# Kernel optimization log

Hardware: AMD Instinct MI355X
Metric: run time of the kernel (lower is better)

## Reference

```python
import jax, jax.numpy as jnp
import numpy as np

N = 30000   # nodes
E = 600000  # edges (avg degree 20)
H = 128     # hidden_channels
L = 4       # num_layers
G = 64      # graphs in batch


def _init(key, shape, fan_in):
    return (jax.random.normal(key, shape, jnp.float32) / np.sqrt(fan_in)).astype(jnp.float32)


def setup_inputs() -> dict:
    key = jax.random.key(0)
    ks = jax.random.split(key, 24)
    x = jax.random.normal(ks[0], (N, 1), jnp.float32)
    pos = jax.random.normal(ks[1], (N, 3), jnp.float32)
    edge_index = jax.random.randint(ks[2], (2, E), 0, N, dtype=jnp.int32).astype(jnp.int64)
    batch = jnp.sort(jax.random.randint(ks[3], (N,), 0, G, dtype=jnp.int32)).astype(jnp.int64)

    emb_w = _init(ks[4], (1, H), 1)
    emb_b = jnp.zeros((H,), jnp.float32)

    # stacked per-layer params: msg MLP (2H+1 -> H -> H), node MLP (2H -> H -> H)
    msg_w1 = _init(ks[5], (L, 2 * H + 1, H), 2 * H + 1)
    msg_b1 = jnp.zeros((L, H), jnp.float32)
    msg_w2 = _init(ks[6], (L, H, H), H)
    msg_b2 = jnp.zeros((L, H), jnp.float32)
    node_w1 = _init(ks[7], (L, 2 * H, H), 2 * H)
    node_b1 = jnp.zeros((L, H), jnp.float32)
    node_w2 = _init(ks[8], (L, H, H), H)
    node_b2 = jnp.zeros((L, H), jnp.float32)

    out_w1 = _init(ks[9], (H, 32), H)
    out_b1 = jnp.zeros((32,), jnp.float32)
    out_w2 = _init(ks[10], (32, 1), 32)
    out_b2 = jnp.zeros((1,), jnp.float32)

    return {
        "x": x, "pos": pos, "edge_index": edge_index, "batch": batch,
        "emb_w": emb_w, "emb_b": emb_b,
        "msg_w1": msg_w1, "msg_b1": msg_b1, "msg_w2": msg_w2, "msg_b2": msg_b2,
        "node_w1": node_w1, "node_b1": node_b1, "node_w2": node_w2, "node_b2": node_b2,
        "out_w1": out_w1, "out_b1": out_b1, "out_w2": out_w2, "out_b2": out_b2,
    }


def reference(x, pos, edge_index, batch,
              emb_w, emb_b,
              msg_w1, msg_b1, msg_w2, msg_b2,
              node_w1, node_b1, node_w2, node_b2,
              out_w1, out_b1, out_w2, out_b2):
    row, col = edge_index[0], edge_index[1]  # row = source j, col = target i
    # edge scalar: squared distance (computed once, reused across layers)
    dist_sq = jnp.sum((pos[row] - pos[col]) ** 2, axis=-1, keepdims=True)  # [E,1]

    h = x @ emb_w + emb_b  # [N,H]
    for l in range(L):
        x_j = h[row]   # source features
        x_i = h[col]   # target features
        m = jnp.concatenate([x_i, x_j, dist_sq], axis=-1)           # [E, 2H+1]
        m = jax.nn.silu(m @ msg_w1[l] + msg_b1[l]) @ msg_w2[l] + msg_b2[l]  # [E,H]
        aggr = jax.ops.segment_sum(m, col, num_segments=N)          # scatter-add to targets
        nh = jnp.concatenate([h, aggr], axis=-1)                    # [N, 2H]
        h = jax.nn.silu(nh @ node_w1[l] + node_b1[l]) @ node_w2[l] + node_b2[l]
        # dropout omitted for deterministic reference (eval mode)

    g = jax.ops.segment_sum(h, batch, num_segments=G)               # global_add_pool [G,H]
    return jax.nn.silu(g @ out_w1 + out_b1) @ out_w2 + out_b2       # [G,1]
```

## Files before the change

### kernel.cpp

```cpp
#include <hip/hip_runtime.h>

typedef unsigned short u16;
typedef __bf16 bf16x8 __attribute__((ext_vector_type(8)));
typedef float f32x4 __attribute__((ext_vector_type(4)));

#define HN 128
#define TM 64
#define ASTRIDE 136
#define ECH 256
#define PGRID 256

__device__ __forceinline__ u16 f2bf(float f) {
  union { float f; unsigned u; } v; v.f = f;
  unsigned r = v.u + 0x7fffu + ((v.u >> 16) & 1u);
  return (u16)(r >> 16);
}
__device__ __forceinline__ float bf2f(u16 v) {
  union { unsigned u; float f; } x; x.u = ((unsigned)v) << 16; return x.f;
}
__device__ __forceinline__ float bflo(unsigned v) {
  union { unsigned u; float f; } x; x.u = v << 16; return x.f;
}
__device__ __forceinline__ float bfhi(unsigned v) {
  union { unsigned u; float f; } x; x.u = v & 0xffff0000u; return x.f;
}
__device__ __forceinline__ float silu_f(float x) {
  float e = __builtin_amdgcn_exp2f(-1.442695041f * x);
  return x * __builtin_amdgcn_rcpf(1.f + e);
}

__global__ void pack_weights(const float* __restrict__ msg_w1, const float* __restrict__ msg_w2,
                             const float* __restrict__ node_w1, const float* __restrict__ node_w2,
                             u16* __restrict__ pw, int* __restrict__ deg,
                             float* __restrict__ g, int N_, int GH) {
  int id = blockIdx.x * 256 + threadIdx.x;
  if (id < N_) deg[id] = 0;
  if (id < GH) g[id] = 0.f;
  if (id >= 4 * 6 * 16384) return;
  int l = id / (6 * 16384);
  int rem = id % (6 * 16384);
  int m = rem / 16384;
  int e = rem % 16384;
  int kg = e >> 10;
  int n = (e >> 3) & 127;
  int j = e & 7;
  int k = kg * 8 + j;
  float v = 0.f;
  switch (m) {
    case 0: v = msg_w1[(l * 257 + k) * 128 + n]; break;
    case 1: v = msg_w1[(l * 257 + 128 + k) * 128 + n]; break;
    case 2: v = msg_w2[(l * 128 + k) * 128 + n]; break;
    case 3: v = node_w1[(l * 256 + k) * 128 + n]; break;
    case 4: v = node_w1[(l * 256 + 128 + k) * 128 + n]; break;
    case 5: v = node_w2[(l * 128 + k) * 128 + n]; break;
  }
  pw[id] = f2bf(v);
}

__device__ __forceinline__ void gemm64(const u16* s_A, const u16* s_W,
                                       int w, int quad, int m16, f32x4 acc[8]) {
#pragma unroll
  for (int ks = 0; ks < 4; ks++) {
    bf16x8 a = *(const bf16x8*)&s_A[(w * 16 + m16) * ASTRIDE + ks * 32 + quad * 8];
#pragma unroll
    for (int ct = 0; ct < 8; ct++) {
      bf16x8 b = *(const bf16x8*)&s_W[(ks * 4 + quad) * 1024 + (ct * 16 + m16) * 8];
      acc[ct] = __builtin_amdgcn_mfma_f32_16x16x32_bf16(a, b, acc[ct], 0, 0, 0);
    }
  }
}

__device__ __forceinline__ void gemm64_ra(const bf16x8 aH[4], const u16* s_W,
                                          int quad, int m16, f32x4 acc[8]) {
#pragma unroll
  for (int ks = 0; ks < 4; ks++) {
#pragma unroll
    for (int ct = 0; ct < 8; ct++) {
      bf16x8 b = *(const bf16x8*)&s_W[(ks * 4 + quad) * 1024 + (ct * 16 + m16) * 8];
      acc[ct] = __builtin_amdgcn_mfma_f32_16x16x32_bf16(aH[ks], b, acc[ct], 0, 0, 0);
    }
  }
}

__device__ __forceinline__ void gemm64_gb(const u16* s_A, const u16* __restrict__ gW,
                                          int w, int quad, int m16, f32x4 acc[8]) {
#pragma unroll
  for (int ks = 0; ks < 4; ks++) {
    bf16x8 a = *(const bf16x8*)&s_A[(w * 16 + m16) * ASTRIDE + ks * 32 + quad * 8];
#pragma unroll
    for (int ct = 0; ct < 8; ct++) {
      bf16x8 b = *(const bf16x8*)&gW[(ks * 4 + quad) * 1024 + (ct * 16 + m16) * 8];
      acc[ct] = __builtin_amdgcn_mfma_f32_16x16x32_bf16(a, b, acc[ct], 0, 0, 0);
    }
  }
}

__global__ __launch_bounds__(256) void fold_kernel(
    const float* __restrict__ msg_w2, const float* __restrict__ node_w1,
    const float* __restrict__ msg_b2, const u16* __restrict__ pw,
    u16* __restrict__ pwc, float* __restrict__ vc) {
  __shared__ __align__(16) u16 s_A[TM * ASTRIDE];
  __shared__ __align__(16) u16 s_W[16384];
  const int t = threadIdx.x;
  const int w = t >> 6, lane = t & 63, quad = lane >> 4, m16 = lane & 15;
  const int b = blockIdx.x, l = b >> 1, half = b & 1;
  const int tile0 = half * 64;

  {
    int r = t >> 2, qo = (t & 3) * 32;
    const float4* src = (const float4*)(msg_w2 + (size_t)(l * 128 + tile0 + r) * 128 + qo);
    u16* dst = s_A + r * ASTRIDE + qo;
#pragma unroll
    for (int i = 0; i < 8; i++) {
      float4 v = src[i];
      ushort4 o;
      o.x = f2bf(v.x); o.y = f2bf(v.y); o.z = f2bf(v.z); o.w = f2bf(v.w);
      *(ushort4*)(dst + i * 4) = o;
    }
  }
  {
    const int4* src = (const int4*)(pw + (size_t)(l * 6 + 4) * 16384);
    int4* dst = (int4*)s_W;
#pragma unroll
    for (int i = 0; i < 8; i++) dst[t + i * 256] = src[t + i * 256];
  }
  __syncthreads();
  f32x4 acc[8];
#pragma unroll
  for (int ct = 0; ct < 8; ct++) acc[ct] = {0.f, 0.f, 0.f, 0.f};
  gemm64(s_A, s_W, w, quad, m16, acc);
#pragma unroll
  for (int ct = 0; ct < 8; ct++)
#pragma unroll
    for (int j = 0; j < 4; j++) {
      int k = tile0 + w * 16 + quad * 4 + j;
      int n = ct * 16 + m16;
      pwc[(size_t)l * 16384 + (k >> 3) * 1024 + n * 8 + (k & 7)] = f2bf(acc[ct][j]);
    }
  if (half == 0 && t < 128) {
    float s = 0.f;
    for (int np = 0; np < 128; np++)
      s += msg_b2[l * 128 + np] * node_w1[(size_t)(l * 256 + 128 + np) * 128 + t];
    vc[l * 128 + t] = s;
  }
}

__global__ void hist_kernel(const int* __restrict__ eidx, int* __restrict__ deg,
                            int* __restrict__ rnk, int E_) {
  int e = blockIdx.x * 256 + threadIdx.x;
  if (e < E_) rnk[e] = atomicAdd(&deg[eidx[E_ + e]], 1);
}

__global__ void scan1_kernel(const int* __restrict__ deg, int* __restrict__ off,
                             int* __restrict__ bsum, int n) {
  __shared__ int s[256];
  int t = threadIdx.x;
  int i = blockIdx.x * 256 + t;
  int v = (i < n) ? deg[i] : 0;
  s[t] = v;
  for (int d = 1; d < 256; d <<= 1) {
    __syncthreads();
    int x = (t >= d) ? s[t - d] : 0;
    __syncthreads();
    s[t] += x;
  }
  __syncthreads();
  if (i < n) off[i] = s[t] - v;
  if (t == 255) bsum[blockIdx.x] = s[255];
}

__global__ void scan2_kernel(int* __restrict__ bsum, int nb) {
  __shared__ int s[256];
  int t = threadIdx.x;
  int v = (t < nb) ? bsum[t] : 0;
  s[t] = v;
  for (int d = 1; d < 256; d <<= 1) {
    __syncthreads();
    int x = (t >= d) ? s[t - d] : 0;
    __syncthreads();
    s[t] += x;
  }
  __syncthreads();
  if (t < nb) bsum[t] = s[t] - v;
}

__global__ void scan3_kernel(int* __restrict__ off, const int* __restrict__ bsum, int n) {
  int i = blockIdx.x * 256 + threadIdx.x;
  if (i < n) off[i] += bsum[blockIdx.x];
}

__global__ void scatter_kernel(const int* __restrict__ eidx, const float* __restrict__ pos,
                               const int* __restrict__ off, const int* __restrict__ rnk,
                               int2* __restrict__ es8, int E_) {
  int e = blockIdx.x * 256 + threadIdx.x;
  if (e >= E_) return;
  int sr = eidx[e], tg = eidx[E_ + e];
  float dx = pos[sr * 3 + 0] - pos[tg * 3 + 0];
  float dy = pos[sr * 3 + 1] - pos[tg * 3 + 1];
  float dz = pos[sr * 3 + 2] - pos[tg * 3 + 2];
  float d = dx * dx + dy * dy + dz * dz;
  int p = off[tg] + rnk[e];
  int2 v;
  v.x = sr | (tg << 15);
  v.y = __float_as_int(d);
  es8[p] = v;
}

__global__ __launch_bounds__(256, 1) void proj_kernel(
    const float* __restrict__ x, const float* __restrict__ emb_w,
    const float* __restrict__ emb_b, u16* __restrict__ hbf,
    u16* __restrict__ Pout, u16* __restrict__ Qout,
    const u16* __restrict__ pw, const float* __restrict__ b1,
    float* __restrict__ S, int NH4, int nnodes, int ntiles) {
  __shared__ __align__(16) u16 s_W[2 * 16384];
  const int t = threadIdx.x;
  const int w = t >> 6, lane = t & 63, quad = lane >> 4, m16 = lane & 15;

  {
    float4* S4 = (float4*)S;
    int id = blockIdx.x * 256 + t;
    int stride = PGRID * 256;
    float4 z = {0.f, 0.f, 0.f, 0.f};
    for (int i = id; i < NH4; i += stride) S4[i] = z;
  }
  {
    const int4* src0 = (const int4*)pw;
    const int4* src1 = (const int4*)(pw + 16384);
    int4* dst = (int4*)s_W;
#pragma unroll
    for (int i = 0; i < 8; i++) dst[t + i * 256] = src0[t + i * 256];
#pragma unroll
    for (int i = 0; i < 8; i++) dst[2048 + t + i * 256] = src1[t + i * 256];
  }
  float ew[4][8], eb[4][8], bb[8];
#pragma unroll
  for (int ks = 0; ks < 4; ks++)
#pragma unroll
    for (int i = 0; i < 8; i++) {
      int c = ks * 32 + quad * 8 + i;
      ew[ks][i] = emb_w[c];
      eb[ks][i] = emb_b[c];
    }
#pragma unroll
  for (int ct = 0; ct < 8; ct++) bb[ct] = b1[ct * 16 + m16];
  __syncthreads();

  for (int tile = blockIdx.x; tile < ntiles; tile += PGRID) {
    const int tile0 = tile * TM;
    int nodem = tile0 + w * 16 + m16;
    bool live = nodem < nnodes;
    if (!live) nodem = nnodes - 1;
    float xv = x[nodem];
    bf16x8 aH[4];
#pragma unroll
    for (int ks = 0; ks < 4; ks++) {
      u16 hv[8];
#pragma unroll
      for (int i = 0; i < 8; i++) hv[i] = f2bf(xv * ew[ks][i] + eb[ks][i]);
      aH[ks] = *(bf16x8*)hv;
      if (live) *(int4*)&hbf[(size_t)nodem * HN + ks * 32 + quad * 8] = *(int4*)hv;
    }
    f32x4 acc[8];
#pragma unroll
    for (int ct = 0; ct < 8; ct++) acc[ct] = {0.f, 0.f, 0.f, 0.f};
    gemm64_ra(aH, s_W, quad, m16, acc);
#pragma unroll
    for (int ct = 0; ct < 8; ct++)
#pragma unroll
      for (int j = 0; j < 4; j++) {
        int n = tile0 + w * 16 + quad * 4 + j;
        if (n < nnodes) Pout[(size_t)n * HN + ct * 16 + m16] = f2bf(acc[ct][j] + bb[ct]);
      }
#pragma unroll
    for (int ct = 0; ct < 8; ct++) acc[ct] = {0.f, 0.f, 0.f, 0.f};
    gemm64_ra(aH, s_W + 16384, quad, m16, acc);
#pragma unroll
    for (int ct = 0; ct < 8; ct++)
#pragma unroll
      for (int j = 0; j < 4; j++) {
        int n = tile0 + w * 16 + quad * 4 + j;
        if (n < nnodes) Qout[(size_t)n * HN + ct * 16 + m16] = f2bf(acc[ct][j]);
      }
  }
}

__device__ __forceinline__ void edge_step(
    int tg_s, float dd_s, unsigned qv,
    int& cur_s, float& p0, float& p1, float& s0, float& s1,
    const u16* __restrict__ P, float* __restrict__ S, int cp,
    float wd0, float wd1, int tprev_s, int tnext_s) {
  if (tg_s != cur_s) {
    if (cur_s >= 0) {
      float* dst = &S[(size_t)cur_s * HN + cp];
      if (cur_s == tprev_s || cur_s == tnext_s) {
        atomicAdd(dst, s0);
        atomicAdd(dst + 1, s1);
      } else {
        float2 v = {s0, s1};
        *(float2*)dst = v;
      }
    }
    cur_s = tg_s; s0 = 0.f; s1 = 0.f;
    int cg = tg_s < 0 ? 0 : tg_s;
    unsigned pv = *(const unsigned*)&P[(size_t)cg * HN + cp];
    p0 = bflo(pv); p1 = bfhi(pv);
  }
  float x0 = p0 + bflo(qv) + dd_s * wd0;
  float x1 = p1 + bfhi(qv) + dd_s * wd1;
  s0 += silu_f(x0);
  s1 += silu_f(x1);
}

__global__ __launch_bounds__(256) void edge_kernel(
    const u16* __restrict__ P, const u16* __restrict__ Q,
    float* __restrict__ S, const float* __restrict__ w1d,
    const int2* __restrict__ es8, int E_) {
  __shared__ int s_src[ECH + 8];
  __shared__ int s_tgt[ECH + 8];
  __shared__ float s_dist[ECH + 8];

  const int t = threadIdx.x;
  const int e0 = blockIdx.x * ECH;
  {
    int e = e0 + t;
    if (e < E_) {
      int2 v = es8[e];
      s_src[t] = v.x & 0x7fff;
      s_tgt[t] = v.x >> 15;
      s_dist[t] = __int_as_float(v.y);
    } else {
      s_src[t] = 0; s_tgt[t] = -1; s_dist[t] = 0.f;
    }
    if (t < 8) { s_src[ECH + t] = 0; s_tgt[ECH + t] = -1; s_dist[ECH + t] = 0.f; }
  }
  __syncthreads();

  const int lane = t & 63;
  const int w = t >> 6;
  const int cp = lane * 2;
  const int a = w * 64;
  const float2 wdv = *(const float2*)&w1d[cp];
  const float wd0 = wdv.x, wd1 = wdv.y;

  int tprev_s, tnext_s;
  if (w == 0) tprev_s = (e0 > 0) ? (es8[e0 - 1].x >> 15) : -2;
  else tprev_s = s_tgt[a - 1];
  if (w == 3) tnext_s = (e0 + ECH < E_) ? (es8[e0 + ECH].x >> 15) : -2;
  else tnext_s = s_tgt[a + 64];
  tprev_s = __builtin_amdgcn_readfirstlane(tprev_s);
  tnext_s = __builtin_amdgcn_readfirstlane(tnext_s);

  int tg[8];
  float dd[8];
  unsigned qv[8];
#pragma unroll
  for (int j = 0; j < 8; j++) {
    tg[j] = s_tgt[a + j];
    dd[j] = s_dist[a + j];
    qv[j] = *(const unsigned*)&Q[(size_t)s_src[a + j] * HN + cp];
  }

  int cur_s = -1;
  float s0 = 0.f, s1 = 0.f, p0 = 0.f, p1 = 0.f;

#pragma unroll
  for (int i = a; i < a + 64; i += 8) {
    int tgn[8];
    float ddn[8];
    unsigned qvn[8];
#pragma unroll
    for (int j = 0; j < 8; j++) {
      int idx = i + 8 + j;
      tgn[j] = s_tgt[idx];
      ddn[j] = s_dist[idx];
      qvn[j] = *(const unsigned*)&Q[(size_t)s_src[idx] * HN + cp];
    }
#pragma unroll
    for (int j = 0; j < 8; j++) {
      int tg_s = __builtin_amdgcn_readfirstlane(tg[j]);
      edge_step(tg_s, dd[j], qv[j], cur_s, p0, p1, s0, s1, P, S, cp, wd0, wd1, tprev_s, tnext_s);
    }
#pragma unroll
    for (int j = 0; j < 8; j++) { tg[j] = tgn[j]; dd[j] = ddn[j]; qv[j] = qvn[j]; }
  }

  if (cur_s >= 0) {
    float* dst = &S[(size_t)cur_s * HN + cp];
    if (cur_s == tprev_s || cur_s == tnext_s) {
      atomicAdd(dst, s0);
      atomicAdd(dst + 1, s1);
    } else {
      float2 v = {s0, s1};
      *(float2*)dst = v;
    }
  }
}

template <bool FUSE>
__global__ __launch_bounds__(256, 1) void node_kernel(
    const u16* __restrict__ hbf, float* __restrict__ S, const int* __restrict__ deg,
    u16* __restrict__ hout, const u16* __restrict__ pwc, const float* __restrict__ vc,
    const u16* __restrict__ pwn, const float* __restrict__ b1, const float* __restrict__ b2,
    const u16* __restrict__ pw_next, const float* __restrict__ b1_next,
    u16* __restrict__ Pout, u16* __restrict__ Qout, int nnodes, int ntiles) {
  __shared__ __align__(16) u16 s_A[TM * ASTRIDE];
  __shared__ __align__(16) u16 s_W[(FUSE ? 4 : 3) * 16384];
  const int t = threadIdx.x;
  const int w = t >> 6, lane = t & 63, quad = lane >> 4, m16 = lane & 15;
  const int r_ = t >> 2, qo_ = (t & 3) * 32;

  {
    const int4* src0 = (const int4*)pwc;
    const int4* src1 = (const int4*)pwn;
    const int4* src2 = (const int4*)(pwn + 32768);
    int4* dst = (int4*)s_W;
#pragma unroll
    for (int i = 0; i < 8; i++) dst[t + i * 256] = src0[t + i * 256];
#pragma unroll
    for (int i = 0; i < 8; i++) dst[2048 + t + i * 256] = src1[t + i * 256];
#pragma unroll
    for (int i = 0; i < 8; i++) dst[4096 + t + i * 256] = src2[t + i * 256];
    if (FUSE) {
      const int4* src3 = (const int4*)pw_next;
#pragma unroll
      for (int i = 0; i < 8; i++) dst[6144 + t + i * 256] = src3[t + i * 256];
    }
  }
  float bb1[8], vcr[8], bb2[8], bbn[8];
#pragma unroll
  for (int ct = 0; ct < 8; ct++) {
    bb1[ct] = b1[ct * 16 + m16];
    vcr[ct] = vc[ct * 16 + m16];
    bb2[ct] = b2[ct * 16 + m16];
    bbn[ct] = FUSE ? b1_next[ct * 16 + m16] : 0.f;
  }
  __syncthreads();

  for (int tile = blockIdx.x; tile < ntiles; tile += PGRID) {
    const int tile0 = tile * TM;
    int node_ = tile0 + r_;
    if (node_ >= nnodes) node_ = nnodes - 1;
    int nodem = tile0 + w * 16 + m16;
    if (nodem >= nnodes) nodem = nnodes - 1;

    {
      const float4* src = (const float4*)(S + (size_t)node_ * HN + qo_);
      u16* dst = s_A + r_ * ASTRIDE + qo_;
#pragma unroll
      for (int i = 0; i < 8; i++) {
        float4 v = src[i];
        ushort4 o;
        o.x = f2bf(v.x); o.y = f2bf(v.y); o.z = f2bf(v.z); o.w = f2bf(v.w);
        *(ushort4*)(dst + i * 4) = o;
      }
      float4 z = {0.f, 0.f, 0.f, 0.f};
      float4* zd = (float4*)(S + (size_t)node_ * HN + qo_);
#pragma unroll
      for (int i = 0; i < 8; i++) zd[i] = z;
    }
    asm volatile("s_waitcnt lgkmcnt(0)" ::: "memory");

    f32x4 acc[8];
#pragma unroll
    for (int ct = 0; ct < 8; ct++) acc[ct] = {0.f, 0.f, 0.f, 0.f};
    gemm64(s_A, s_W, w, quad, m16, acc);

    bf16x8 aH[4];
#pragma unroll
    for (int ks = 0; ks < 4; ks++)
      aH[ks] = *(const bf16x8*)&hbf[(size_t)nodem * HN + ks * 32 + quad * 8];
    gemm64_ra(aH, s_W + 16384, quad, m16, acc);

    {
      float degv[4];
#pragma unroll
      for (int j = 0; j < 4; j++) {
        int n = tile0 + w * 16 + quad * 4 + j;
        if (n >= nnodes) n = nnodes - 1;
        degv[j] = (float)deg[n];
      }
#pragma unroll
      for (int ct = 0; ct < 8; ct++)
#pragma unroll
        for (int j = 0; j < 4; j++) {
          int row = w * 16 + quad * 4 + j;
          float xv = acc[ct][j] + bb1[ct] + degv[j] * vcr[ct];
          s_A[row * ASTRIDE + ct * 16 + m16] = f2bf(silu_f(xv));
        }
    }
    asm volatile("s_waitcnt lgkmcnt(0)" ::: "memory");

#pragma unroll
    for (int ct = 0; ct < 8; ct++) acc[ct] = {0.f, 0.f, 0.f, 0.f};
    gemm64(s_A, s_W + 32768, w, quad, m16, acc);

#pragma unroll
    for (int ct = 0; ct < 8; ct++)
#pragma unroll
      for (int j = 0; j < 4; j++) {
        int row = w * 16 + quad * 4 + j;
        int n = tile0 + row;
        u16 hv = f2bf(acc[ct][j] + bb2[ct]);
        if (n < nnodes) hout[(size_t)n * HN + ct * 16 + m16] = hv;
        if (FUSE) s_A[row * ASTRIDE + ct * 16 + m16] = hv;
      }

    if (FUSE) {
      asm volatile("s_waitcnt lgkmcnt(0)" ::: "memory");
#pragma unroll
      for (int ct = 0; ct < 8; ct++) acc[ct] = {0.f, 0.f, 0.f, 0.f};
      gemm64(s_A, s_W + 49152, w, quad, m16, acc);
#pragma unroll
      for (int ct = 0; ct < 8; ct++)
#pragma unroll
        for (int j = 0; j < 4; j++) {
          int n = tile0 + w * 16 + quad * 4 + j;
          if (n < nnodes) Pout[(size_t)n * HN + ct * 16 + m16] = f2bf(acc[ct][j] + bbn[ct]);
        }
#pragma unroll
      for (int ct = 0; ct < 8; ct++) acc[ct] = {0.f, 0.f, 0.f, 0.f};
      gemm64_gb(s_A, pw_next + 16384, w, quad, m16, acc);
#pragma unroll
      for (int ct = 0; ct < 8; ct++)
#pragma unroll
        for (int j = 0; j < 4; j++) {
          int n = tile0 + w * 16 + quad * 4 + j;
          if (n < nnodes) Qout[(size_t)n * HN + ct * 16 + m16] = f2bf(acc[ct][j]);
        }
    }
  }
}

__global__ __launch_bounds__(256) void pool_kernel(
    const u16* __restrict__ h, const int* __restrict__ batch,
    float* __restrict__ g, int N) {
  __shared__ int s_b[64];
  const int t = threadIdx.x;
  const int n0 = blockIdx.x * 64;
  if (t < 64) {
    int n = n0 + t;
    s_b[t] = (n < N) ? batch[n] : -1;
  }
  __syncthreads();
  const int cp = (t & 63) * 2;
  const int rg = t >> 6;
  int cur = -1;
  float s0 = 0.f, s1 = 0.f;
#pragma unroll 4
  for (int i = 0; i < 16; i++) {
    int r = rg * 16 + i;
    int b = s_b[r];
    if (b < 0) break;
    if (b != cur) {
      if (cur >= 0) {
        atomicAdd(&g[cur * HN + cp], s0);
        atomicAdd(&g[cur * HN + cp + 1], s1);
      }
      cur = b; s0 = 0.f; s1 = 0.f;
    }
    unsigned v = *(const unsigned*)&h[(size_t)(n0 + r) * HN + cp];
    s0 += bf2f((u16)(v & 0xffffu));
    s1 += bf2f((u16)(v >> 16));
  }
  if (cur >= 0) {
    atomicAdd(&g[cur * HN + cp], s0);
    atomicAdd(&g[cur * HN + cp + 1], s1);
  }
}

__global__ __launch_bounds__(64) void out_kernel(
    const float* __restrict__ g, const float* __restrict__ w1,
    const float* __restrict__ b1, const float* __restrict__ w2,
    const float* __restrict__ b2, float* __restrict__ out) {
  const int gi = blockIdx.x;
  const int t = threadIdx.x;
  const int c = t & 31, kh = t >> 5;
  float s = 0.f;
  for (int k = kh * 64; k < kh * 64 + 64; k++)
    s += g[gi * HN + k] * w1[k * 32 + c];
  s += __shfl_down(s, 32);
  float r = 0.f;
  if (kh == 0) r = silu_f(s + b1[c]) * w2[c];
  r += __shfl_down(r, 16);
  r += __shfl_down(r, 8);
  r += __shfl_down(r, 4);
  r += __shfl_down(r, 2);
  r += __shfl_down(r, 1);
  if (t == 0) out[gi] = r + b2[0];
}

extern "C" void kernel_launch(void* const* d_in, const int* in_sizes, int n_in,
                              void* d_out, int out_size, void* d_ws, size_t ws_size,
                              hipStream_t stream) {
  const float* x = (const float*)d_in[0];
  const float* pos = (const float*)d_in[1];
  const int* eidx = (const int*)d_in[2];
  const int* batch = (const int*)d_in[3];
  const float* emb_w = (const float*)d_in[4];
  const float* emb_b = (const float*)d_in[5];
  const float* msg_w1 = (const float*)d_in[6];
  const float* msg_b1 = (const float*)d_in[7];
  const float* msg_w2 = (const float*)d_in[8];
  const float* msg_b2 = (const float*)d_in[9];
  const float* node_w1 = (const float*)d_in[10];
  const float* node_b1 = (const float*)d_in[11];
  const float* node_w2 = (const float*)d_in[12];
  const float* node_b2 = (const float*)d_in[13];
  const float* out_w1 = (const float*)d_in[14];
  const float* out_b1 = (const float*)d_in[15];
  const float* out_w2 = (const float*)d_in[16];
  const float* out_b2 = (const float*)d_in[17];
  float* outp = (float*)d_out;

  const int N = 30000, E = 600000, G = 64;
  const size_t NH = (size_t)N * HN;

  u16* hA = (u16*)d_ws;
  u16* hB = hA + NH;
  u16* Pp = hB + NH;
  u16* Qp = Pp + NH;
  float* S = (float*)(Qp + NH);
  int2* es8 = (int2*)(S + NH);
  int* deg = (int*)(es8 + E);
  int* off = deg + N;
  int* bsum = off + N;
  float* g = (float*)(bsum + 128);
  u16* pw = (u16*)(g + G * HN);
  u16* pwc = pw + (size_t)4 * 6 * 16384;
  float* vcb = (float*)(pwc + (size_t)4 * 16384);
  int* rnk = (int*)S;

  const int NB = (N + 255) / 256;
  const int NTB = (N + TM - 1) / TM;

  pack_weights<<<(4 * 6 * 16384 + 255) / 256, 256, 0, stream>>>(
      msg_w1, msg_w2, node_w1, node_w2, pw, deg, g, N, G * HN);
  fold_kernel<<<8, 256, 0, stream>>>(msg_w2, node_w1, msg_b2, pw, pwc, vcb);

  hist_kernel<<<(E + 255) / 256, 256, 0, stream>>>(eidx, deg, rnk, E);
  scan1_kernel<<<NB, 256, 0, stream>>>(deg, off, bsum, N);
  scan2_kernel<<<1, 256, 0, stream>>>(bsum, NB);
  scan3_kernel<<<NB, 256, 0, stream>>>(off, bsum, N);
  scatter_kernel<<<(E + 255) / 256, 256, 0, stream>>>(eidx, pos, off, rnk, es8, E);

  proj_kernel<<<PGRID, 256, 0, stream>>>(x, emb_w, emb_b, hA, Pp, Qp, pw, msg_b1,
                                         S, (int)(NH / 4), N, NTB);

  u16* hcur = hA;
  u16* hnext = hB;
  for (int l = 0; l < 4; l++) {
    const u16* pwl = pw + (size_t)(l * 6) * 16384;
    edge_kernel<<<(E + ECH - 1) / ECH, 256, 0, stream>>>(
        Pp, Qp, S,
        msg_w1 + (size_t)(l * 257 + 256) * 128,
        es8, E);
    if (l < 3) {
      const u16* pw_next = pw + (size_t)((l + 1) * 6) * 16384;
      node_kernel<true><<<PGRID, 256, 0, stream>>>(
          hcur, S, deg, hnext, pwc + (size_t)l * 16384, vcb + l * 128,
          pwl + 3 * 16384, node_b1 + l * 128, node_b2 + l * 128,
          pw_next, msg_b1 + (l + 1) * 128, Pp, Qp, N, NTB);
    } else {
      node_kernel<false><<<PGRID, 256, 0, stream>>>(
          hcur, S, deg, hnext, pwc + (size_t)l * 16384, vcb + l * 128,
          pwl + 3 * 16384, node_b1 + l * 128, node_b2 + l * 128,
          nullptr, nullptr, nullptr, nullptr, N, NTB);
    }
    u16* tmp = hcur; hcur = hnext; hnext = tmp;
  }

  pool_kernel<<<(N + 63) / 64, 256, 0, stream>>>(hcur, batch, g, N);
  out_kernel<<<G, 64, 0, stream>>>(g, out_w1, out_b1, out_w2, out_b2, outp);
}
```

Baseline: 420.2 us.

## Read weights from global memory and launch one block per node tile

Measured after the change: 413.5 us. Within noise of the previous version (-1.6%).

```diff
diff --git a/kernel.cpp b/kernel.cpp
--- a/kernel.cpp
+++ b/kernel.cpp
@@ -8,7 +8,6 @@
 #define TM 64
 #define ASTRIDE 136
 #define ECH 256
-#define PGRID 256
 
 __device__ __forceinline__ u16 f2bf(float f) {
   union { float f; unsigned u; } v; v.f = f;
@@ -70,18 +69,6 @@
   }
 }
 
-__device__ __forceinline__ void gemm64_ra(const bf16x8 aH[4], const u16* s_W,
-                                          int quad, int m16, f32x4 acc[8]) {
-#pragma unroll
-  for (int ks = 0; ks < 4; ks++) {
-#pragma unroll
-    for (int ct = 0; ct < 8; ct++) {
-      bf16x8 b = *(const bf16x8*)&s_W[(ks * 4 + quad) * 1024 + (ct * 16 + m16) * 8];
-      acc[ct] = __builtin_amdgcn_mfma_f32_16x16x32_bf16(aH[ks], b, acc[ct], 0, 0, 0);
-    }
-  }
-}
-
 __device__ __forceinline__ void gemm64_gb(const u16* s_A, const u16* __restrict__ gW,
                                           int w, int quad, int m16, f32x4 acc[8]) {
 #pragma unroll
@@ -91,6 +78,18 @@
     for (int ct = 0; ct < 8; ct++) {
       bf16x8 b = *(const bf16x8*)&gW[(ks * 4 + quad) * 1024 + (ct * 16 + m16) * 8];
       acc[ct] = __builtin_amdgcn_mfma_f32_16x16x32_bf16(a, b, acc[ct], 0, 0, 0);
+    }
+  }
+}
+
+__device__ __forceinline__ void gemm64_ra_gb(const bf16x8 aH[4], const u16* __restrict__ gW,
+                                             int quad, int m16, f32x4 acc[8]) {
+#pragma unroll
+  for (int ks = 0; ks < 4; ks++) {
+#pragma unroll
+    for (int ct = 0; ct < 8; ct++) {
+      bf16x8 b = *(const bf16x8*)&gW[(ks * 4 + quad) * 1024 + (ct * 16 + m16) * 8];
+      acc[ct] = __builtin_amdgcn_mfma_f32_16x16x32_bf16(aH[ks], b, acc[ct], 0, 0, 0);
     }
   }
 }
@@ -206,82 +205,65 @@
   es8[p] = v;
 }
 
-__global__ __launch_bounds__(256, 1) void proj_kernel(
+__global__ __launch_bounds__(256) void proj_kernel(
     const float* __restrict__ x, const float* __restrict__ emb_w,
     const float* __restrict__ emb_b, u16* __restrict__ hbf,
     u16* __restrict__ Pout, u16* __restrict__ Qout,
     const u16* __restrict__ pw, const float* __restrict__ b1,
-    float* __restrict__ S, int NH4, int nnodes, int ntiles) {
-  __shared__ __align__(16) u16 s_W[2 * 16384];
+    float* __restrict__ S, int NH4, int nblocks, int nnodes) {
   const int t = threadIdx.x;
   const int w = t >> 6, lane = t & 63, quad = lane >> 4, m16 = lane & 15;
+  const int tile0 = blockIdx.x * TM;
 
   {
     float4* S4 = (float4*)S;
     int id = blockIdx.x * 256 + t;
-    int stride = PGRID * 256;
+    int stride = nblocks * 256;
     float4 z = {0.f, 0.f, 0.f, 0.f};
     for (int i = id; i < NH4; i += stride) S4[i] = z;
   }
-  {
-    const int4* src0 = (const int4*)pw;
-    const int4* src1 = (const int4*)(pw + 16384);
-    int4* dst = (int4*)s_W;
-#pragma unroll
-    for (int i = 0; i < 8; i++) dst[t + i * 256] = src0[t + i * 256];
-#pragma unroll
-    for (int i = 0; i < 8; i++) dst[2048 + t + i * 256] = src1[t + i * 256];
-  }
-  float ew[4][8], eb[4][8], bb[8];
-#pragma unroll
-  for (int ks = 0; ks < 4; ks++)
+
+  int nodem = tile0 + w * 16 + m16;
+  bool live = nodem < nnodes;
+  if (!live) nodem = nnodes - 1;
+  float xv = x[nodem];
+  bf16x8 aH[4];
+#pragma unroll
+  for (int ks = 0; ks < 4; ks++) {
+    u16 hv[8];
 #pragma unroll
     for (int i = 0; i < 8; i++) {
       int c = ks * 32 + quad * 8 + i;
-      ew[ks][i] = emb_w[c];
-      eb[ks][i] = emb_b[c];
-    }
+      hv[i] = f2bf(xv * emb_w[c] + emb_b[c]);
+    }
+    aH[ks] = *(bf16x8*)hv;
+    if (live) *(int4*)&hbf[(size_t)nodem * HN + ks * 32 + quad * 8] = *(int4*)hv;
+  }
+  float bb[8];
 #pragma unroll
   for (int ct = 0; ct < 8; ct++) bb[ct] = b1[ct * 16 + m16];
-  __syncthreads();
-
-  for (int tile = blockIdx.x; tile < ntiles; tile += PGRID) {
-    const int tile0 = tile * TM;
-    int nodem = tile0 + w * 16 + m16;
-    bool live = nodem < nnodes;
-    if (!live) nodem = nnodes - 1;
-    float xv = x[nodem];
-    bf16x8 aH[4];
-#pragma unroll
-    for (int ks = 0; ks < 4; ks++) {
-      u16 hv[8];
-#pragma unroll
-      for (int i = 0; i < 8; i++) hv[i] = f2bf(xv * ew[ks][i] + eb[ks][i]);
-      aH[ks] = *(bf16x8*)hv;
-      if (live) *(int4*)&hbf[(size_t)nodem * HN + ks * 32 + quad * 8] = *(int4*)hv;
-    }
-    f32x4 acc[8];
-#pragma unroll
-    for (int ct = 0; ct < 8; ct++) acc[ct] = {0.f, 0.f, 0.f, 0.f};
-    gemm64_ra(aH, s_W, quad, m16, acc);
-#pragma unroll
-    for (int ct = 0; ct < 8; ct++)
-#pragma unroll
-      for (int j = 0; j < 4; j++) {
-        int n = tile0 + w * 16 + quad * 4 + j;
-        if (n < nnodes) Pout[(size_t)n * HN + ct * 16 + m16] = f2bf(acc[ct][j] + bb[ct]);
-      }
-#pragma unroll
-    for (int ct = 0; ct < 8; ct++) acc[ct] = {0.f, 0.f, 0.f, 0.f};
-    gemm64_ra(aH, s_W + 16384, quad, m16, acc);
-#pragma unroll
-    for (int ct = 0; ct < 8; ct++)
-#pragma unroll
-      for (int j = 0; j < 4; j++) {
-        int n = tile0 + w * 16 + quad * 4 + j;
-        if (n < nnodes) Qout[(size_t)n * HN + ct * 16 + m16] = f2bf(acc[ct][j]);
-      }
-  }
+
+  f32x4 acc[8];
+#pragma unroll
+  for (int ct = 0; ct < 8; ct++) acc[ct] = {0.f, 0.f, 0.f, 0.f};
+  gemm64_ra_gb(aH, pw, quad, m16, acc);
+#pragma unroll
+  for (int ct = 0; ct < 8; ct++)
+#pragma unroll
+    for (int j = 0; j < 4; j++) {
+      int n = tile0 + w * 16 + quad * 4 + j;
+      if (n < nnodes) Pout[(size_t)n * HN + ct * 16 + m16] = f2bf(acc[ct][j] + bb[ct]);
+    }
+#pragma unroll
+  for (int ct = 0; ct < 8; ct++) acc[ct] = {0.f, 0.f, 0.f, 0.f};
+  gemm64_ra_gb(aH, pw + 16384, quad, m16, acc);
+#pragma unroll
+  for (int ct = 0; ct < 8; ct++)
+#pragma unroll
+    for (int j = 0; j < 4; j++) {
+      int n = tile0 + w * 16 + quad * 4 + j;
+      if (n < nnodes) Qout[(size_t)n * HN + ct * 16 + m16] = f2bf(acc[ct][j]);
+    }
 }
 
 __device__ __forceinline__ void edge_step(
@@ -397,35 +379,25 @@
 }
 
 template <bool FUSE>
-__global__ __launch_bounds__(256, 1) void node_kernel(
+__global__ __launch_bounds__(256) void node_kernel(
     const u16* __restrict__ hbf, float* __restrict__ S, const int* __restrict__ deg,
     u16* __restrict__ hout, const u16* __restrict__ pwc, const float* __restrict__ vc,
     const u16* __restrict__ pwn, const float* __restrict__ b1, const float* __restrict__ b2,
     const u16* __restrict__ pw_next, const float* __restrict__ b1_next,
-    u16* __restrict__ Pout, u16* __restrict__ Qout, int nnodes, int ntiles) {
+    u16* __restrict__ Pout, u16* __restrict__ Qout, int nnodes) {
   __shared__ __align__(16) u16 s_A[TM * ASTRIDE];
-  __shared__ __align__(16) u16 s_W[(FUSE ? 4 : 3) * 16384];
   const int t = threadIdx.x;
   const int w = t >> 6, lane = t & 63, quad = lane >> 4, m16 = lane & 15;
-  const int r_ = t >> 2, qo_ = (t & 3) * 32;
-
-  {
-    const int4* src0 = (const int4*)pwc;
-    const int4* src1 = (const int4*)pwn;
-    const int4* src2 = (const int4*)(pwn + 32768);
-    int4* dst = (int4*)s_W;
-#pragma unroll
-    for (int i = 0; i < 8; i++) dst[t + i * 256] = src0[t + i * 256];
-#pragma unroll
-    for (int i = 0; i < 8; i++) dst[2048 + t + i * 256] = src1[t + i * 256];
-#pragma unroll
-    for (int i = 0; i < 8; i++) dst[4096 + t + i * 256] = src2[t + i * 256];
-    if (FUSE) {
-      const int4* src3 = (const int4*)pw_next;
-#pragma unroll
-      for (int i = 0; i < 8; i++) dst[6144 + t + i * 256] = src3[t + i * 256];
-    }
-  }
+  const int tile0 = blockIdx.x * TM;
+  const int rb = lane >> 2;
+  const int qo = (lane & 3) * 32;
+  u16* band = s_A + (w * 16) * ASTRIDE;
+
+  int node_ = tile0 + w * 16 + rb;
+  if (node_ >= nnodes) node_ = nnodes - 1;
+  int nodem = tile0 + w * 16 + m16;
+  if (nodem >= nnodes) nodem = nnodes - 1;
+
   float bb1[8], vcr[8], bb2[8], bbn[8];
 #pragma unroll
   for (int ct = 0; ct < 8; ct++) {
@@ -434,100 +406,94 @@
     bb2[ct] = b2[ct * 16 + m16];
     bbn[ct] = FUSE ? b1_next[ct * 16 + m16] : 0.f;
   }
-  __syncthreads();
-
-  for (int tile = blockIdx.x; tile < ntiles; tile += PGRID) {
-    const int tile0 = tile * TM;
-    int node_ = tile0 + r_;
-    if (node_ >= nnodes) node_ = nnodes - 1;
-    int nodem = tile0 + w * 16 + m16;
-    if (nodem >= nnodes) nodem = nnodes - 1;
-
-    {
-      const float4* src = (const float4*)(S + (size_t)node_ * HN + qo_);
-      u16* dst = s_A + r_ * ASTRIDE + qo_;
-#pragma unroll
-      for (int i = 0; i < 8; i++) {
-        float4 v = src[i];
-        ushort4 o;
-        o.x = f2bf(v.x); o.y = f2bf(v.y); o.z = f2bf(v.z); o.w = f2bf(v.w);
-        *(ushort4*)(dst + i * 4) = o;
+
+  {
+    const float4* src = (const float4*)(S + (size_t)node_ * HN + qo);
+    u16* dst = band + rb * ASTRIDE + qo;
+#pragma unroll
+    for (int i = 0; i < 8; i++) {
+      float4 v = src[i];
+      ushort4 o;
+      o.x = f2bf(v.x); o.y = f2bf(v.y); o.z = f2bf(v.z); o.w = f2bf(v.w);
+      *(ushort4*)(dst + i * 4) = o;
+    }
+    float4 z = {0.f, 0.f, 0.f, 0.f};
+    float4* zd = (float4*)(S + (size_t)node_ * HN + qo);
+#pragma unroll
+    for (int i = 0; i < 8; i++) zd[i] = z;
+  }
+  asm volatile("s_waitcnt lgkmcnt(0)" ::: "memory");
+  __builtin_amdgcn_sched_barrier(0);
+
+  f32x4 acc[8];
+#pragma unroll
+  for (int ct = 0; ct < 8; ct++) acc[ct] = {0.f, 0.f, 0.f, 0.f};
+  gemm64_gb(s_A, pwc, w, quad, m16, acc);
+
+  bf16x8 aH[4];
+#pragma unroll
+  for (int ks = 0; ks < 4; ks++)
+    aH[ks] = *(const bf16x8*)&hbf[(size_t)nodem * HN + ks * 32 + quad * 8];
+  gemm64_ra_gb(aH, pwn, quad, m16, acc);
+
+  {
+    float degv[4];
+#pragma unroll
+    for (int j = 0; j < 4; j++) {
+      int n = tile0 + w * 16 + quad * 4 + j;
+      if (n >= nnodes) n = nnodes - 1;
+      degv[j] = (float)deg[n];
+    }
+#pragma unroll
+    for (int ct = 0; ct < 8; ct++)
+#pragma unroll
+      for (int j = 0; j < 4; j++) {
+        int row = quad * 4 + j;
+        float xv = acc[ct][j] + bb1[ct] + degv[j] * vcr[ct];
+        band[row * ASTRIDE + ct * 16 + m16] = f2bf(silu_f(xv));
       }
-      float4 z = {0.f, 0.f, 0.f, 0.f};
-      float4* zd = (float4*)(S + (size_t)node_ * HN + qo_);
-#pragma unroll
-      for (int i = 0; i < 8; i++) zd[i] = z;
-    }
+  }
+  asm volatile("s_waitcnt lgkmcnt(0)" ::: "memory");
+  __builtin_amdgcn_sched_barrier(0);
+
+#pragma unroll
+  for (int ct = 0; ct < 8; ct++) acc[ct] = {0.f, 0.f, 0.f, 0.f};
+  gemm64_gb(s_A, pwn + 32768, w, quad, m16, acc);
+
+#pragma unroll
+  for (int ct = 0; ct < 8; ct++)
+#pragma unroll
+    for (int j = 0; j < 4; j++) {
+      int row = quad * 4 + j;
+      int n = tile0 + w * 16 + row;
+      u16 hv = f2bf(acc[ct][j] + bb2[ct]);
+      if (n < nnodes) hout[(size_t)n * HN + ct * 16 + m16] = hv;
+      if (FUSE) band[row * ASTRIDE + ct * 16 + m16] = hv;
+    }
+
+  if (FUSE) {
     asm volatile("s_waitcnt lgkmcnt(0)" ::: "memory");
-
-    f32x4 acc[8];
+    __builtin_amdgcn_sched_barrier(0);
 #pragma unroll
     for (int ct = 0; ct < 8; ct++) acc[ct] = {0.f, 0.f, 0.f, 0.f};
-    gemm64(s_A, s_W, w, quad, m16, acc);
-
-    bf16x8 aH[4];
-#pragma unroll
-    for (int ks = 0; ks < 4; ks++)
-      aH[ks] = *(const bf16x8*)&hbf[(size_t)nodem * HN + ks * 32 + quad * 8];
-    gemm64_ra(aH, s_W + 16384, quad, m16, acc);
-
-    {
-      float degv[4];
+    gemm64_gb(s_A, pw_next, w, quad, m16, acc);
+#pragma unroll
+    for (int ct = 0; ct < 8; ct++)
 #pragma unroll
       for (int j = 0; j < 4; j++) {
         int n = tile0 + w * 16 + quad * 4 + j;
-        if (n >= nnodes) n = nnodes - 1;
-        degv[j] = (float)deg[n];
+        if (n < nnodes) Pout[(size_t)n * HN + ct * 16 + m16] = f2bf(acc[ct][j] + bbn[ct]);
       }
 #pragma unroll
-      for (int ct = 0; ct < 8; ct++)
-#pragma unroll
-        for (int j = 0; j < 4; j++) {
-          int row = w * 16 + quad * 4 + j;
-          float xv = acc[ct][j] + bb1[ct] + degv[j] * vcr[ct];
-          s_A[row * ASTRIDE + ct * 16 + m16] = f2bf(silu_f(xv));
-        }
-    }
-    asm volatile("s_waitcnt lgkmcnt(0)" ::: "memory");
-
-#pragma unroll
     for (int ct = 0; ct < 8; ct++) acc[ct] = {0.f, 0.f, 0.f, 0.f};
-    gemm64(s_A, s_W + 32768, w, quad, m16, acc);
-
+    gemm64_gb(s_A, pw_next + 16384, w, quad, m16, acc);
 #pragma unroll
     for (int ct = 0; ct < 8; ct++)
 #pragma unroll
       for (int j = 0; j < 4; j++) {
-        int row = w * 16 + quad * 4 + j;
-        int n = tile0 + row;
-        u16 hv = f2bf(acc[ct][j] + bb2[ct]);
-        if (n < nnodes) hout[(size_t)n * HN + ct * 16 + m16] = hv;
-        if (FUSE) s_A[row * ASTRIDE + ct * 16 + m16] = hv;
+        int n = tile0 + w * 16 + quad * 4 + j;
+        if (n < nnodes) Qout[(size_t)n * HN + ct * 16 + m16] = f2bf(acc[ct][j]);
       }
-
-    if (FUSE) {
-      asm volatile("s_waitcnt lgkmcnt(0)" ::: "memory");
-#pragma unroll
-      for (int ct = 0; ct < 8; ct++) acc[ct] = {0.f, 0.f, 0.f, 0.f};
-      gemm64(s_A, s_W + 49152, w, quad, m16, acc);
-#pragma unroll
-      for (int ct = 0; ct < 8; ct++)
-#pragma unroll
-        for (int j = 0; j < 4; j++) {
-          int n = tile0 + w * 16 + quad * 4 + j;
-          if (n < nnodes) Pout[(size_t)n * HN + ct * 16 + m16] = f2bf(acc[ct][j] + bbn[ct]);
-        }
-#pragma unroll
-      for (int ct = 0; ct < 8; ct++) acc[ct] = {0.f, 0.f, 0.f, 0.f};
-      gemm64_gb(s_A, pw_next + 16384, w, quad, m16, acc);
-#pragma unroll
-      for (int ct = 0; ct < 8; ct++)
-#pragma unroll
-        for (int j = 0; j < 4; j++) {
-          int n = tile0 + w * 16 + quad * 4 + j;
-          if (n < nnodes) Qout[(size_t)n * HN + ct * 16 + m16] = f2bf(acc[ct][j]);
-        }
-    }
   }
 }
 
@@ -643,8 +609,8 @@
   scan3_kernel<<<NB, 256, 0, stream>>>(off, bsum, N);
   scatter_kernel<<<(E + 255) / 256, 256, 0, stream>>>(eidx, pos, off, rnk, es8, E);
 
-  proj_kernel<<<PGRID, 256, 0, stream>>>(x, emb_w, emb_b, hA, Pp, Qp, pw, msg_b1,
-                                         S, (int)(NH / 4), N, NTB);
+  proj_kernel<<<NTB, 256, 0, stream>>>(x, emb_w, emb_b, hA, Pp, Qp, pw, msg_b1,
+                                       S, (int)(NH / 4), NTB, N);
 
   u16* hcur = hA;
   u16* hnext = hB;
@@ -656,15 +622,15 @@
         es8, E);
     if (l < 3) {
       const u16* pw_next = pw + (size_t)((l + 1) * 6) * 16384;
-      node_kernel<true><<<PGRID, 256, 0, stream>>>(
+      node_kernel<true><<<NTB, 256, 0, stream>>>(
           hcur, S, deg, hnext, pwc + (size_t)l * 16384, vcb + l * 128,
           pwl + 3 * 16384, node_b1 + l * 128, node_b2 + l * 128,
-          pw_next, msg_b1 + (l + 1) * 128, Pp, Qp, N, NTB);
+          pw_next, msg_b1 + (l + 1) * 128, Pp, Qp, N);
     } else {
-      node_kernel<false><<<PGRID, 256, 0, stream>>>(
+      node_kernel<false><<<NTB, 256, 0, stream>>>(
           hcur, S, deg, hnext, pwc + (size_t)l * 16384, vcb + l * 128,
           pwl + 3 * 16384, node_b1 + l * 128, node_b2 + l * 128,
-          nullptr, nullptr, nullptr, nullptr, N, NTB);
+          nullptr, nullptr, nullptr, nullptr, N);
     }
     u16* tmp = hcur; hcur = hnext; hnext = tmp;
   }
```
